# Kernel tuning notes

Hardware: AMD Instinct MI355X
Metric: run time of the kernel (lower is better)

The kernel has to match this reference:

```python
import jax, jax.numpy as jnp
import numpy as np

L = 4          # decomposition_levels
PRUNE_Q = 0.4  # pruning_ratio


def haar_dwt2(img):
    a = img[:, 0::2, 0::2]; b = img[:, 0::2, 1::2]
    c = img[:, 1::2, 0::2]; d = img[:, 1::2, 1::2]
    cA = (a + b + c + d) * 0.5
    cH = (a - b + c - d) * 0.5
    cV = (a + b - c - d) * 0.5
    cD = (a - b - c + d) * 0.5
    return cA, cH, cV, cD


def haar_idwt2(cA, cH, cV, cD):
    # exact inverse of haar_dwt2: [B, h, w] -> [B, 2h, 2w]
    a = (cA + cH + cV + cD) * 0.5
    b = (cA - cH + cV - cD) * 0.5
    c = (cA + cH - cV - cD) * 0.5
    d = (cA - cH - cV + cD) * 0.5
    B, h, w = cA.shape
    top = jnp.stack([a, b], axis=-1).reshape(B, h, 2 * w)  # interleave cols
    bot = jnp.stack([c, d], axis=-1).reshape(B, h, 2 * w)
    return jnp.stack([top, bot], axis=2).reshape(B, 2 * h, 2 * w)  # interleave rows


def setup_inputs() -> dict:
    key = jax.random.key(0)
    k1, k2, k3 = jax.random.split(key, 3)
    B, in_dim, out_dim = 128, 4096, 4096
    x = jax.random.normal(k1, (B, in_dim), jnp.float32)
    base_weight = jax.random.normal(k2, (out_dim, in_dim), jnp.float32) * 0.02
    bias = jax.random.normal(k3, (out_dim,), jnp.float32) * 0.02
    scale_factors = jnp.ones((L, 4), jnp.float32)  # per-level, per-subband
    return {"x": x, "base_weight": base_weight, "bias": bias,
            "scale_factors": scale_factors}


def reference(x, base_weight, bias, scale_factors):
    B, in_dim = x.shape
    S = int(np.sqrt(in_dim))  # 64: each sample viewed as SxS image
    base_out = x @ base_weight.T  # [B, out_dim]

    # multi-level Haar analysis with per-level scaling + quantile pruning
    cA = x.reshape(B, S, S)
    levels = []
    for l in range(L):
        cA, cH, cV, cD = haar_dwt2(cA)
        co = jnp.stack([cA, cH, cV, cD], axis=1)  # [B, 4, h, w]
        co = co * scale_factors[l][None, :, None, None]
        ab = jnp.abs(co)
        thr = jnp.quantile(ab, PRUNE_Q, axis=-1, keepdims=True)
        co = co * (ab > thr).astype(co.dtype)
        levels.append(co)

    # synthesis from pruned coefficients
    rec = levels[-1][:, 0]  # coarsest pruned cA
    for l in range(L - 1, -1, -1):
        rec = haar_idwt2(rec, levels[l][:, 1], levels[l][:, 2], levels[l][:, 3])

    wavelet_out = rec.reshape(B, in_dim)  # out_dim == in_dim
    return base_out + wavelet_out + bias
```

## Files before the change

### kernel.cpp

```cpp
#include <hip/hip_runtime.h>
#include <hip/hip_bf16.h>

typedef __attribute__((ext_vector_type(8))) short bf16x8;
typedef __attribute__((ext_vector_type(4))) float f32x4;

__device__ __forceinline__ unsigned short f2bf(float f) {
  unsigned int u = __float_as_uint(f);
  u += 0x7FFFu + ((u >> 16) & 1u);
  return (unsigned short)(u >> 16);
}

__device__ __forceinline__ bf16x8 pack8(float4 lo, float4 hi) {
  union { unsigned int u[4]; bf16x8 v; } r;
  asm("v_cvt_pk_bf16_f32 %0, %1, %2" : "=v"(r.u[0]) : "v"(lo.x), "v"(lo.y));
  asm("v_cvt_pk_bf16_f32 %0, %1, %2" : "=v"(r.u[1]) : "v"(lo.z), "v"(lo.w));
  asm("v_cvt_pk_bf16_f32 %0, %1, %2" : "=v"(r.u[2]) : "v"(hi.x), "v"(hi.y));
  asm("v_cvt_pk_bf16_f32 %0, %1, %2" : "=v"(r.u[3]) : "v"(hi.z), "v"(hi.w));
  return r.v;
}

__host__ __device__ constexpr int prOffset(int l) {
  return (l == 0) ? 0 : (l == 1) ? 3072 : (l == 2) ? 3840 : 4032;
}

template<int L>
__device__ __forceinline__ void level_fwd(float* cur, float* tmp, float* ab,
                                          float* pr, float* thrL, float* thrH,
                                          const float* __restrict__ scl, int tid) {
  constexpr int HALF = 32 >> L, LOG2 = 5 - L, HH = HALF * HALF, TOT = 4 * HH;
  constexpr int H = HALF * 2;
  constexpr float P = 0.4f * (float)(HALF - 1);
  constexpr int K = (int)P;
  constexpr float FRAC = P - (float)K;
  const float s0 = scl[4 * L + 0], s1 = scl[4 * L + 1];
  const float s2 = scl[4 * L + 2], s3 = scl[4 * L + 3];
  for (int e = tid; e < HH; e += 256) {
    const int i = e >> LOG2, j = e & (HALF - 1);
    const float a = cur[(i * 2) * H + j * 2];
    const float b = cur[(i * 2) * H + j * 2 + 1];
    const float c = cur[(i * 2 + 1) * H + j * 2];
    const float d = cur[(i * 2 + 1) * H + j * 2 + 1];
    tmp[e]          = (((a + b) + c) + d) * 0.5f;
    tmp[HH + e]     = (((a - b) + c) - d) * 0.5f;
    tmp[2 * HH + e] = (((a + b) - c) - d) * 0.5f;
    tmp[3 * HH + e] = (((a - b) - c) + d) * 0.5f;
  }
  __syncthreads();
  for (int e = tid; e < TOT; e += 256) {
    const int s = e >> (2 * LOG2);
    const float sc = (s < 2) ? (s == 0 ? s0 : s1) : (s == 2 ? s2 : s3);
    ab[e] = fabsf(tmp[e] * sc);
  }
  __syncthreads();
  constexpr int CH = (TOT >= 256) ? TOT / 256 : 1;
  {
    const int base = tid * CH;
    if (base < TOT) {
      const int rowbase = base & ~(HALF - 1);
      float v[CH]; int clt[CH], ceq[CH];
#pragma unroll
      for (int c = 0; c < CH; ++c) { v[c] = ab[base + c]; clt[c] = 0; ceq[c] = 0; }
#pragma unroll
      for (int rr = 0; rr < HALF; ++rr) {
        const float a = ab[rowbase + rr];
#pragma unroll
        for (int c = 0; c < CH; ++c) {
          clt[c] += (a < v[c]) ? 1 : 0;
          ceq[c] += (a == v[c]) ? 1 : 0;
        }
      }
      const int row = base >> LOG2;
#pragma unroll
      for (int c = 0; c < CH; ++c) {
        if (clt[c] <= K && K < clt[c] + ceq[c]) thrL[row] = v[c];
        if (clt[c] <= K + 1 && K + 1 < clt[c] + ceq[c]) thrH[row] = v[c];
      }
    }
  }
  __syncthreads();
  for (int e = tid; e < TOT; e += 256) {
    const int s = e >> (2 * LOG2);
    const int row = e >> LOG2;
    const float sc = (s < 2) ? (s == 0 ? s0 : s1) : (s == 2 ? s2 : s3);
    const float thr = thrL[row] * (1.0f - FRAC) + thrH[row] * FRAC;
    const float co = tmp[e] * sc;
    const float val = (fabsf(co) > thr) ? co : 0.0f;
    if (s >= 1) pr[prOffset(L) + e - HH] = val;
    else {
      if (L == 3) pr[4080 + e] = val;
      cur[e] = tmp[e];
    }
  }
  __syncthreads();
}

__global__ __launch_bounds__(256) void wavelet_kernel(
    const float* __restrict__ x, const float* __restrict__ bias,
    const float* __restrict__ scl, float* __restrict__ out,
    unsigned short* __restrict__ xb, int writeXb) {
  __shared__ float sh[16384];
  float* cur = sh;
  float* tmp = sh + 4096;
  float* ab  = sh + 8192;
  float* pr  = sh + 12288;
  float* thrL = cur + 2048;
  float* thrH = cur + 2176;
  const int b = blockIdx.x, tid = threadIdx.x;
  const float* xi = x + (size_t)b * 4096;

  for (int i = tid; i < 4096; i += 256) {
    const float v = xi[i];
    cur[i] = v;
    if (writeXb) xb[(size_t)b * 4096 + i] = f2bf(v);
  }
  __syncthreads();

  level_fwd<0>(cur, tmp, ab, pr, thrL, thrH, scl, tid);
  level_fwd<1>(cur, tmp, ab, pr, thrL, thrH, scl, tid);
  level_fwd<2>(cur, tmp, ab, pr, thrL, thrH, scl, tid);
  level_fwd<3>(cur, tmp, ab, pr, thrL, thrH, scl, tid);

#pragma unroll
  for (int l = 3; l >= 0; --l) {
    const int half = 64 >> (l + 1);
    const int hh = half * half;
    const int po = prOffset(l);
    const float* src = (l == 3) ? &pr[4080] : ((l & 1) ? tmp : cur);
    float* dst = (l & 1) ? cur : tmp;
    const int W2 = half * 2;
    for (int e = tid; e < hh; e += 256) {
      const int i = e / half, j = e - i * half;
      const float cA = src[e];
      const float cH = pr[po + 0 * hh + i * half + j];
      const float cV = pr[po + 1 * hh + i * half + j];
      const float cD = pr[po + 2 * hh + i * half + j];
      const float a2 = (((cA + cH) + cV) + cD) * 0.5f;
      const float b2 = (((cA - cH) + cV) - cD) * 0.5f;
      const float c2 = (((cA + cH) - cV) - cD) * 0.5f;
      const float d2 = (((cA - cH) - cV) + cD) * 0.5f;
      dst[(i * 2) * W2 + j * 2]         = a2;
      dst[(i * 2) * W2 + j * 2 + 1]     = b2;
      dst[(i * 2 + 1) * W2 + j * 2]     = c2;
      dst[(i * 2 + 1) * W2 + j * 2 + 1] = d2;
    }
    __syncthreads();
  }
  float* o = out + (size_t)b * 4096;
  for (int e = tid; e < 4096; e += 256) o[e] = tmp[e] + bias[e];
}

__global__ __launch_bounds__(256, 2) void gemm_ws(
    const unsigned short* __restrict__ xb, const float* __restrict__ w,
    float* __restrict__ out) {
  const int tid = threadIdx.x, lane = tid & 63, wv = tid >> 6;
  const int fr = lane & 15, k8 = (lane >> 4) * 8;
  const int nt = blockIdx.x & 63, ks = blockIdx.x >> 6;
  const int n0 = nt * 64, k0 = ks * 512;
  const float* wr = w + (size_t)(n0 + wv * 16 + fr) * 4096 + k0 + k8;
  const unsigned short* xr = xb + (size_t)fr * 4096 + k0 + k8;

  f32x4 acc[8];
#pragma unroll
  for (int mi = 0; mi < 8; ++mi) acc[mi] = f32x4{0.f, 0.f, 0.f, 0.f};

  float4 bfr[4][2];
  bf16x8 afr[2][8];
#pragma unroll
  for (int p = 0; p < 4; ++p) {
    bfr[p][0] = *(const float4*)(wr + p * 32);
    bfr[p][1] = *(const float4*)(wr + p * 32 + 4);
  }
#pragma unroll
  for (int p = 0; p < 2; ++p)
#pragma unroll
    for (int mi = 0; mi < 8; ++mi)
      afr[p][mi] = *(const bf16x8*)(xr + mi * 16 * 4096 + p * 32);

#pragma unroll
  for (int t = 0; t < 16; ++t) {
    const bf16x8 bb = pack8(bfr[t & 3][0], bfr[t & 3][1]);
#pragma unroll
    for (int mi = 0; mi < 8; ++mi)
      acc[mi] = __builtin_amdgcn_mfma_f32_16x16x32_bf16(afr[t & 1][mi], bb,
                                                        acc[mi], 0, 0, 0);
    if (t < 12) {
      bfr[t & 3][0] = *(const float4*)(wr + (t + 4) * 32);
      bfr[t & 3][1] = *(const float4*)(wr + (t + 4) * 32 + 4);
    }
    if (t < 14) {
#pragma unroll
      for (int mi = 0; mi < 8; ++mi)
        afr[t & 1][mi] = *(const bf16x8*)(xr + mi * 16 * 4096 + (t + 2) * 32);
    }
  }

  const int rq = (lane >> 4) * 4;
  const int col = n0 + wv * 16 + fr;
#pragma unroll
  for (int mi = 0; mi < 8; ++mi)
#pragma unroll
    for (int j = 0; j < 4; ++j)
      atomicAdd(&out[(size_t)(mi * 16 + rq + j) * 4096 + col], acc[mi][j]);
}

__global__ __launch_bounds__(256, 2) void gemm_kernel(
    const float* __restrict__ x, const float* __restrict__ w,
    float* __restrict__ out) {
  __shared__ __align__(16) unsigned short Asm[2][128][40];
  __shared__ __align__(16) unsigned short Bsm[2][64][40];
  const int tid = threadIdx.x;
  const int nt = blockIdx.x & 63, ks = blockIdx.x >> 6;
  const int n0 = nt * 64, k0 = ks * 512;
  const int q = tid & 7, r0 = tid >> 3;
  const int lane = tid & 63, wid = tid >> 6;
  const int wm = wid >> 1, wn = wid & 1;
  const int fr = lane & 15, k8 = (lane >> 4) * 8;

  f32x4 acc[4][2];
#pragma unroll
  for (int mi = 0; mi < 4; ++mi)
#pragma unroll
    for (int ni = 0; ni < 2; ++ni) acc[mi][ni] = f32x4{0.f, 0.f, 0.f, 0.f};

  float4 ra[4]; float4 rb[2];
#pragma unroll
  for (int p = 0; p < 4; ++p)
    ra[p] = *(const float4*)&x[(size_t)(r0 + p * 32) * 4096 + k0 + q * 4];
#pragma unroll
  for (int p = 0; p < 2; ++p)
    rb[p] = *(const float4*)&w[(size_t)(n0 + r0 + p * 32) * 4096 + k0 + q * 4];
#pragma unroll
  for (int p = 0; p < 4; ++p) {
    ushort4 pk = {f2bf(ra[p].x), f2bf(ra[p].y), f2bf(ra[p].z), f2bf(ra[p].w)};
    *(ushort4*)&Asm[0][r0 + p * 32][q * 4] = pk;
  }
#pragma unroll
  for (int p = 0; p < 2; ++p) {
    ushort4 pk = {f2bf(rb[p].x), f2bf(rb[p].y), f2bf(rb[p].z), f2bf(rb[p].w)};
    *(ushort4*)&Bsm[0][r0 + p * 32][q * 4] = pk;
  }
  __syncthreads();

  for (int t = 0; t < 16; ++t) {
    const int cb = t & 1;
    if (t < 15) {
      const int kg = k0 + (t + 1) * 32;
#pragma unroll
      for (int p = 0; p < 4; ++p)
        ra[p] = *(const float4*)&x[(size_t)(r0 + p * 32) * 4096 + kg + q * 4];
#pragma unroll
      for (int p = 0; p < 2; ++p)
        rb[p] = *(const float4*)&w[(size_t)(n0 + r0 + p * 32) * 4096 + kg + q * 4];
    }
    bf16x8 af[4], bg[2];
#pragma unroll
    for (int mi = 0; mi < 4; ++mi)
      af[mi] = *(const bf16x8*)&Asm[cb][wm * 64 + mi * 16 + fr][k8];
#pragma unroll
    for (int ni = 0; ni < 2; ++ni)
      bg[ni] = *(const bf16x8*)&Bsm[cb][wn * 32 + ni * 16 + fr][k8];
#pragma unroll
    for (int mi = 0; mi < 4; ++mi)
#pragma unroll
      for (int ni = 0; ni < 2; ++ni)
        acc[mi][ni] = __builtin_amdgcn_mfma_f32_16x16x32_bf16(af[mi], bg[ni],
                                                              acc[mi][ni], 0, 0, 0);
    if (t < 15) {
#pragma unroll
      for (int p = 0; p < 4; ++p) {
        ushort4 pk = {f2bf(ra[p].x), f2bf(ra[p].y), f2bf(ra[p].z), f2bf(ra[p].w)};
        *(ushort4*)&Asm[cb ^ 1][r0 + p * 32][q * 4] = pk;
      }
#pragma unroll
      for (int p = 0; p < 2; ++p) {
        ushort4 pk = {f2bf(rb[p].x), f2bf(rb[p].y), f2bf(rb[p].z), f2bf(rb[p].w)};
        *(ushort4*)&Bsm[cb ^ 1][r0 + p * 32][q * 4] = pk;
      }
    }
    __syncthreads();
  }

  const int rbase = wm * 64 + (lane >> 4) * 4;
  const int cbase = n0 + wn * 32 + fr;
#pragma unroll
  for (int mi = 0; mi < 4; ++mi)
#pragma unroll
    for (int ni = 0; ni < 2; ++ni)
#pragma unroll
      for (int j = 0; j < 4; ++j)
        atomicAdd(&out[(size_t)(rbase + mi * 16 + j) * 4096 + cbase + ni * 16],
                  acc[mi][ni][j]);
}

extern "C" void kernel_launch(void* const* d_in, const int* in_sizes, int n_in,
                              void* d_out, int out_size, void* d_ws, size_t ws_size,
                              hipStream_t stream) {
  const float* x    = (const float*)d_in[0];
  const float* w    = (const float*)d_in[1];
  const float* bias = (const float*)d_in[2];
  const float* scl  = (const float*)d_in[3];
  float* out = (float*)d_out;
  const bool useWs = ws_size >= (size_t)128 * 4096 * 2;
  unsigned short* xbp = (unsigned short*)d_ws;
  hipLaunchKernelGGL(wavelet_kernel, dim3(128), dim3(256), 0, stream,
                     x, bias, scl, out, xbp, useWs ? 1 : 0);
  if (useWs)
    hipLaunchKernelGGL(gemm_ws, dim3(512), dim3(256), 0, stream, xbp, w, out);
  else
    hipLaunchKernelGGL(gemm_kernel, dim3(512), dim3(256), 0, stream, x, w, out);
}
```

Baseline: 153.5 us.

## Stage GEMM tiles via direct global-to-LDS loads and widen wavelet kernel to 512 threads

Replaces the register-streaming bf16 GEMM with a version that stages swizzled A and B tiles into LDS through global_load_lds with double buffering, halves the K slice per block and doubles the grid to 1024 blocks. The wavelet kernel moves to 512 threads, fuses the abs/scale pass into the forward Haar loop to drop one barrier, and vectorizes input/output with float4. Together these aim to raise memory-level parallelism and occupancy. The cost is twice as many atomic adds to the output and extra LDS traffic and barriers per K step.

```diff
diff --git a/kernel.cpp b/kernel.cpp
--- a/kernel.cpp
+++ b/kernel.cpp
@@ -17,6 +17,12 @@
   asm("v_cvt_pk_bf16_f32 %0, %1, %2" : "=v"(r.u[2]) : "v"(hi.x), "v"(hi.y));
   asm("v_cvt_pk_bf16_f32 %0, %1, %2" : "=v"(r.u[3]) : "v"(hi.z), "v"(hi.w));
   return r.v;
+}
+
+__device__ __forceinline__ void gload16(const void* g, void* l) {
+  __builtin_amdgcn_global_load_lds(
+      (const __attribute__((address_space(1))) void*)g,
+      (__attribute__((address_space(3))) void*)l, 16, 0, 0);
 }
 
 __host__ __device__ constexpr int prOffset(int l) {
@@ -34,25 +40,23 @@
   constexpr float FRAC = P - (float)K;
   const float s0 = scl[4 * L + 0], s1 = scl[4 * L + 1];
   const float s2 = scl[4 * L + 2], s3 = scl[4 * L + 3];
-  for (int e = tid; e < HH; e += 256) {
+  for (int e = tid; e < HH; e += 512) {
     const int i = e >> LOG2, j = e & (HALF - 1);
     const float a = cur[(i * 2) * H + j * 2];
     const float b = cur[(i * 2) * H + j * 2 + 1];
     const float c = cur[(i * 2 + 1) * H + j * 2];
     const float d = cur[(i * 2 + 1) * H + j * 2 + 1];
-    tmp[e]          = (((a + b) + c) + d) * 0.5f;
-    tmp[HH + e]     = (((a - b) + c) - d) * 0.5f;
-    tmp[2 * HH + e] = (((a + b) - c) - d) * 0.5f;
-    tmp[3 * HH + e] = (((a - b) - c) + d) * 0.5f;
-  }
-  __syncthreads();
-  for (int e = tid; e < TOT; e += 256) {
-    const int s = e >> (2 * LOG2);
-    const float sc = (s < 2) ? (s == 0 ? s0 : s1) : (s == 2 ? s2 : s3);
-    ab[e] = fabsf(tmp[e] * sc);
-  }
-  __syncthreads();
-  constexpr int CH = (TOT >= 256) ? TOT / 256 : 1;
+    const float vA = (((a + b) + c) + d) * 0.5f;
+    const float vH = (((a - b) + c) - d) * 0.5f;
+    const float vV = (((a + b) - c) - d) * 0.5f;
+    const float vD = (((a - b) - c) + d) * 0.5f;
+    tmp[e]          = vA;  ab[e]          = fabsf(vA * s0);
+    tmp[HH + e]     = vH;  ab[HH + e]     = fabsf(vH * s1);
+    tmp[2 * HH + e] = vV;  ab[2 * HH + e] = fabsf(vV * s2);
+    tmp[3 * HH + e] = vD;  ab[3 * HH + e] = fabsf(vD * s3);
+  }
+  __syncthreads();
+  constexpr int CH = (TOT >= 512) ? TOT / 512 : 1;
   {
     const int base = tid * CH;
     if (base < TOT) {
@@ -78,7 +82,7 @@
     }
   }
   __syncthreads();
-  for (int e = tid; e < TOT; e += 256) {
+  for (int e = tid; e < TOT; e += 512) {
     const int s = e >> (2 * LOG2);
     const int row = e >> LOG2;
     const float sc = (s < 2) ? (s == 0 ? s0 : s1) : (s == 2 ? s2 : s3);
@@ -94,7 +98,7 @@
   __syncthreads();
 }
 
-__global__ __launch_bounds__(256) void wavelet_kernel(
+__global__ __launch_bounds__(512) void wavelet_kernel(
     const float* __restrict__ x, const float* __restrict__ bias,
     const float* __restrict__ scl, float* __restrict__ out,
     unsigned short* __restrict__ xb, int writeXb) {
@@ -108,10 +112,13 @@
   const int b = blockIdx.x, tid = threadIdx.x;
   const float* xi = x + (size_t)b * 4096;
 
-  for (int i = tid; i < 4096; i += 256) {
-    const float v = xi[i];
-    cur[i] = v;
-    if (writeXb) xb[(size_t)b * 4096 + i] = f2bf(v);
+  for (int i = tid; i < 1024; i += 512) {
+    const float4 v = ((const float4*)xi)[i];
+    *(float4*)&cur[i * 4] = v;
+    if (writeXb) {
+      ushort4 pk = {f2bf(v.x), f2bf(v.y), f2bf(v.z), f2bf(v.w)};
+      *(ushort4*)&xb[(size_t)b * 4096 + i * 4] = pk;
+    }
   }
   __syncthreads();
 
@@ -128,7 +135,7 @@
     const float* src = (l == 3) ? &pr[4080] : ((l & 1) ? tmp : cur);
     float* dst = (l & 1) ? cur : tmp;
     const int W2 = half * 2;
-    for (int e = tid; e < hh; e += 256) {
+    for (int e = tid; e < hh; e += 512) {
       const int i = e / half, j = e - i * half;
       const float cA = src[e];
       const float cH = pr[po + 0 * hh + i * half + j];
@@ -146,56 +153,73 @@
     __syncthreads();
   }
   float* o = out + (size_t)b * 4096;
-  for (int e = tid; e < 4096; e += 256) o[e] = tmp[e] + bias[e];
-}
-
-__global__ __launch_bounds__(256, 2) void gemm_ws(
+  const float4* t4 = (const float4*)tmp;
+  const float4* b4 = (const float4*)bias;
+  for (int i = tid; i < 1024; i += 512) {
+    float4 t = t4[i], bb = b4[i];
+    float4 r = {t.x + bb.x, t.y + bb.y, t.z + bb.z, t.w + bb.w};
+    ((float4*)o)[i] = r;
+  }
+}
+
+__global__ __launch_bounds__(256, 4) void gemm_v4(
     const unsigned short* __restrict__ xb, const float* __restrict__ w,
     float* __restrict__ out) {
+  __shared__ __align__(16) unsigned short A_lds[2][128 * 32];
+  __shared__ __align__(16) float B_lds[2][64 * 32];
   const int tid = threadIdx.x, lane = tid & 63, wv = tid >> 6;
-  const int fr = lane & 15, k8 = (lane >> 4) * 8;
+  const int fr = lane & 15, kq = lane >> 4;
   const int nt = blockIdx.x & 63, ks = blockIdx.x >> 6;
-  const int n0 = nt * 64, k0 = ks * 512;
-  const float* wr = w + (size_t)(n0 + wv * 16 + fr) * 4096 + k0 + k8;
-  const unsigned short* xr = xb + (size_t)fr * 4096 + k0 + k8;
+  const int n0 = nt * 64, k0 = ks * 256;
+
+  const int sA0 = tid, sA1 = 256 + tid;
+  const int rA0 = sA0 >> 2, cA0 = (sA0 & 3) ^ ((rA0 >> 1) & 3);
+  const int rA1 = sA1 >> 2, cA1 = (sA1 & 3) ^ ((rA1 >> 1) & 3);
+  const unsigned short* aSrc0 = xb + (size_t)rA0 * 4096 + k0 + cA0 * 8;
+  const unsigned short* aSrc1 = xb + (size_t)rA1 * 4096 + k0 + cA1 * 8;
+  const int rB0 = sA0 >> 3, cB0 = (sA0 & 7) ^ (rB0 & 7);
+  const int rB1 = sA1 >> 3, cB1 = (sA1 & 7) ^ (rB1 & 7);
+  const float* bSrc0 = w + (size_t)(n0 + rB0) * 4096 + k0 + cB0 * 4;
+  const float* bSrc1 = w + (size_t)(n0 + rB1) * 4096 + k0 + cB1 * 4;
 
   f32x4 acc[8];
 #pragma unroll
   for (int mi = 0; mi < 8; ++mi) acc[mi] = f32x4{0.f, 0.f, 0.f, 0.f};
 
-  float4 bfr[4][2];
-  bf16x8 afr[2][8];
-#pragma unroll
-  for (int p = 0; p < 4; ++p) {
-    bfr[p][0] = *(const float4*)(wr + p * 32);
-    bfr[p][1] = *(const float4*)(wr + p * 32 + 4);
-  }
-#pragma unroll
-  for (int p = 0; p < 2; ++p)
-#pragma unroll
-    for (int mi = 0; mi < 8; ++mi)
-      afr[p][mi] = *(const bf16x8*)(xr + mi * 16 * 4096 + p * 32);
-
-#pragma unroll
-  for (int t = 0; t < 16; ++t) {
-    const bf16x8 bb = pack8(bfr[t & 3][0], bfr[t & 3][1]);
-#pragma unroll
-    for (int mi = 0; mi < 8; ++mi)
-      acc[mi] = __builtin_amdgcn_mfma_f32_16x16x32_bf16(afr[t & 1][mi], bb,
-                                                        acc[mi], 0, 0, 0);
-    if (t < 12) {
-      bfr[t & 3][0] = *(const float4*)(wr + (t + 4) * 32);
-      bfr[t & 3][1] = *(const float4*)(wr + (t + 4) * 32 + 4);
-    }
-    if (t < 14) {
-#pragma unroll
-      for (int mi = 0; mi < 8; ++mi)
-        afr[t & 1][mi] = *(const bf16x8*)(xr + mi * 16 * 4096 + (t + 2) * 32);
-    }
-  }
-
-  const int rq = (lane >> 4) * 4;
+  const int aslot = kq ^ ((fr >> 1) & 3);
+  const int R2 = wv * 16 + fr;
+  const int bo0 = R2 * 128 + (((kq * 2 + 0) ^ (R2 & 7)) * 16);
+  const int bo1 = R2 * 128 + (((kq * 2 + 1) ^ (R2 & 7)) * 16);
+
+  auto STAGE = [&](int buf, int t) {
+    gload16(aSrc0 + t * 32, (char*)&A_lds[buf][0] + tid * 16);
+    gload16(aSrc1 + t * 32, (char*)&A_lds[buf][0] + (256 + tid) * 16);
+    gload16(bSrc0 + t * 32, (char*)&B_lds[buf][0] + tid * 16);
+    gload16(bSrc1 + t * 32, (char*)&B_lds[buf][0] + (256 + tid) * 16);
+  };
+
+  STAGE(0, 0);
+  __syncthreads();
+  int cur = 0;
+#pragma unroll
+  for (int t = 0; t < 8; ++t) {
+    if (t < 7) STAGE(cur ^ 1, t + 1);
+    const char* Ab = (const char*)&A_lds[cur][0];
+    const char* Bb = (const char*)&B_lds[cur][0];
+    const float4 b0 = *(const float4*)(Bb + bo0);
+    const float4 b1 = *(const float4*)(Bb + bo1);
+    const bf16x8 bb = pack8(b0, b1);
+#pragma unroll
+    for (int mi = 0; mi < 8; ++mi) {
+      const bf16x8 af = *(const bf16x8*)(Ab + (mi * 16 + fr) * 64 + aslot * 16);
+      acc[mi] = __builtin_amdgcn_mfma_f32_16x16x32_bf16(af, bb, acc[mi], 0, 0, 0);
+    }
+    __syncthreads();
+    cur ^= 1;
+  }
+
   const int col = n0 + wv * 16 + fr;
+  const int rq = kq * 4;
 #pragma unroll
   for (int mi = 0; mi < 8; ++mi)
 #pragma unroll
@@ -302,10 +326,10 @@
   float* out = (float*)d_out;
   const bool useWs = ws_size >= (size_t)128 * 4096 * 2;
   unsigned short* xbp = (unsigned short*)d_ws;
-  hipLaunchKernelGGL(wavelet_kernel, dim3(128), dim3(256), 0, stream,
+  hipLaunchKernelGGL(wavelet_kernel, dim3(128), dim3(512), 0, stream,
                      x, bias, scl, out, xbp, useWs ? 1 : 0);
   if (useWs)
-    hipLaunchKernelGGL(gemm_ws, dim3(512), dim3(256), 0, stream, xbp, w, out);
+    hipLaunchKernelGGL(gemm_v4, dim3(1024), dim3(256), 0, stream, xbp, w, out);
   else
     hipLaunchKernelGGL(gemm_kernel, dim3(512), dim3(256), 0, stream, x, w, out);
 }
```

New measurement: 135.6 us. 1.13x faster.
